# Performance work log

Measured on AMD Instinct MI355X. Metric: run time of the kernel, lower is better.

The kernel has to match this reference:

```python
import jax, jax.numpy as jnp
import numpy as np

B, S, D_IN, D_OUT, H = 4, 2048, 1024, 1024, 16
HD = D_OUT // H


def setup_inputs() -> dict:
    key = jax.random.key(0)
    ks = jax.random.split(key, 6)
    s = 1.0 / np.sqrt(D_IN)
    x = jax.random.normal(ks[0], (B, S, D_IN), dtype=jnp.float32)
    Wq = jax.random.uniform(ks[1], (D_OUT, D_IN), jnp.float32, -s, s)  # torch Linear weight [out,in]
    Wk = jax.random.uniform(ks[2], (D_OUT, D_IN), jnp.float32, -s, s)
    Wv = jax.random.uniform(ks[3], (D_OUT, D_IN), jnp.float32, -s, s)
    so = 1.0 / np.sqrt(D_OUT)
    Wo = jax.random.uniform(ks[4], (D_OUT, D_OUT), jnp.float32, -so, so)
    bo = jax.random.uniform(ks[5], (D_OUT,), jnp.float32, -so, so)
    return {"x": x, "Wq": Wq, "Wk": Wk, "Wv": Wv, "Wo": Wo, "bo": bo}


def reference(x, Wq, Wk, Wv, Wo, bo):
    b, n, _ = x.shape
    # projections (torch Linear: x @ W^T), split heads -> [b, h, n, hd]
    def heads(y):
        return y.reshape(b, n, H, HD).transpose(0, 2, 1, 3)
    q = heads(x @ Wq.T)
    k = heads(x @ Wk.T)
    v = heads(x @ Wv.T)
    scores = jnp.einsum('bhqd,bhkd->bhqk', q, k)
    causal = jnp.triu(jnp.ones((n, n), dtype=bool), k=1)
    scores = jnp.where(causal, -jnp.inf, scores)
    attn = jax.nn.softmax(scores / np.sqrt(HD), axis=-1)  # dropout p=0.0 -> identity
    ctx = jnp.einsum('bhqk,bhkd->bhqd', attn, v)
    ctx = ctx.transpose(0, 2, 1, 3).reshape(b, n, D_OUT)
    return ctx @ Wo.T + bo
```

## Files before the change

kernel.cpp:

```cpp
#include <hip/hip_runtime.h>
#include <hip/hip_bf16.h>
#include <stdint.h>

#define B_N 4
#define SEQ 2048
#define DMODEL 1024
#define NHEAD 16
#define HDIM 64
#define BHEADS (B_N * NHEAD)
#define MROWS (B_N * SEQ)

typedef short bf16x8_t __attribute__((ext_vector_type(8)));
typedef float f32x4_t __attribute__((ext_vector_type(4)));

static __device__ __forceinline__ unsigned short f2bf(float f) {
  __hip_bfloat16 h = __float2bfloat16(f);
  return __builtin_bit_cast(unsigned short, h);
}

#define GLDS16(gp, lp)                                                        \
  __builtin_amdgcn_global_load_lds(                                           \
      (const __attribute__((address_space(1))) unsigned int*)(gp),            \
      (__attribute__((address_space(3))) unsigned int*)(lp), 16, 0, 0)

__global__ void cast_f32_bf16_v4(const float* __restrict__ in,
                                 unsigned short* __restrict__ out, int n4,
                                 float scale) {
  int i = blockIdx.x * blockDim.x + threadIdx.x;
  if (i >= n4) return;
  float4 v = reinterpret_cast<const float4*>(in)[i];
  ushort4 o;
  o.x = f2bf(v.x * scale); o.y = f2bf(v.y * scale);
  o.z = f2bf(v.z * scale); o.w = f2bf(v.w * scale);
  reinterpret_cast<ushort4*>(out)[i] = o;
}

__global__ void cast_weights(const float* __restrict__ Wq,
                             const float* __restrict__ Wk,
                             const float* __restrict__ Wv,
                             const float* __restrict__ Wo,
                             unsigned short* __restrict__ out) {
  int i = blockIdx.x * blockDim.x + threadIdx.x;
  int mat = i >> 18;
  int off = i & 262143;
  const float* src = (mat == 0) ? Wq : (mat == 1) ? Wk : (mat == 2) ? Wv : Wo;
  float scale = (mat == 0) ? 0.125f : 1.0f;
  float4 v = reinterpret_cast<const float4*>(src)[off];
  ushort4 o;
  o.x = f2bf(v.x * scale); o.y = f2bf(v.y * scale);
  o.z = f2bf(v.z * scale); o.w = f2bf(v.w * scale);
  reinterpret_cast<ushort4*>(out)[i] = o;
}

__global__ __launch_bounds__(256, 2)
void gemm_qkv(const unsigned short* __restrict__ A,
              const unsigned short* __restrict__ W,
              unsigned short* __restrict__ Out) {
  __shared__ __align__(16) unsigned short smem[18432];
  unsigned short* As = smem;
  unsigned short* Bs = smem + 4096;

  const int t = threadIdx.x;
  const int lane = t & 63;
  const int w = t >> 6;
  const int quad = lane >> 4;
  const int l16 = lane & 15;
  const int rowBase = blockIdx.x * 128;
  const int colBase = blockIdx.y * 128;
  const int mat = colBase >> 10;
  const int nl = colBase & 1023;
  const int wr = (w >> 1) * 64;
  const int wc = (w & 1) * 64;
  const int K = DMODEL;

  f32x4_t zero4 = {0.f, 0.f, 0.f, 0.f};
  f32x4_t acc[4][4];
#pragma unroll
  for (int i = 0; i < 4; i++)
#pragma unroll
    for (int j = 0; j < 4; j++) acc[i][j] = zero4;

  const int sseg = ((t & 3) ^ ((t >> 3) & 3)) * 8;
  const unsigned short* Ag0 = A + (size_t)(rowBase + (t >> 2)) * K + sseg;
  const unsigned short* Ag1 = A + (size_t)(rowBase + 64 + (t >> 2)) * K + sseg;
  const unsigned short* Bg0 = W + (size_t)(colBase + (t >> 2)) * K + sseg;
  const unsigned short* Bg1 = W + (size_t)(colBase + 64 + (t >> 2)) * K + sseg;
  char* lA0 = (char*)As + t * 16;
  char* lA1 = (char*)As + t * 16 + 4096;
  char* lB0 = (char*)Bs + t * 16;
  char* lB1 = (char*)Bs + t * 16 + 4096;

  const int qsw = (quad ^ ((l16 >> 1) & 3)) * 8;

  for (int k0 = 0; k0 < K; k0 += 32) {
    GLDS16(Ag0 + k0, lA0);
    GLDS16(Ag1 + k0, lA1);
    GLDS16(Bg0 + k0, lB0);
    GLDS16(Bg1 + k0, lB1);
    __syncthreads();

    bf16x8_t af[4], bfr[4];
#pragma unroll
    for (int rt = 0; rt < 4; rt++)
      af[rt] = *(const bf16x8_t*)((const char*)As +
                                  ((wr + rt * 16 + l16) * 32 + qsw) * 2);
#pragma unroll
    for (int ct = 0; ct < 4; ct++)
      bfr[ct] = *(const bf16x8_t*)((const char*)Bs +
                                   ((wc + ct * 16 + l16) * 32 + qsw) * 2);
#pragma unroll
    for (int rt = 0; rt < 4; rt++)
#pragma unroll
      for (int ct = 0; ct < 4; ct++)
        acc[rt][ct] = __builtin_amdgcn_mfma_f32_16x16x32_bf16(
            af[rt], bfr[ct], acc[rt][ct], 0, 0, 0);
    __syncthreads();
  }

  const int hh = (nl + wc) >> 6;
  const int bb = rowBase >> 11;

  if (mat == 2) {
    unsigned short* T = smem + w * 4608;
#pragma unroll
    for (int ct = 0; ct < 4; ct++)
#pragma unroll
      for (int rt = 0; rt < 4; rt++) {
        ushort4 pk;
        pk.x = f2bf(acc[rt][ct][0]);
        pk.y = f2bf(acc[rt][ct][1]);
        pk.z = f2bf(acc[rt][ct][2]);
        pk.w = f2bf(acc[rt][ct][3]);
        *(ushort4*)&T[(ct * 16 + l16) * 72 + rt * 16 + quad * 4] = pk;
      }
    const int srow = (rowBase & (SEQ - 1)) + wr;
    unsigned short* Cq = Out + 2 * (size_t)MROWS * DMODEL;
#pragma unroll
    for (int it = 0; it < 8; it++) {
      int nn = it * 8 + (lane >> 3);
      int sg = lane & 7;
      uint4 d = *(const uint4*)&T[nn * 72 + sg * 8];
      *(uint4*)(Cq + ((size_t)(bb * NHEAD + hh) * HDIM + nn) * SEQ + srow +
                sg * 8) = d;
    }
  } else {
    unsigned short* T = smem + w * 4608;
#pragma unroll
    for (int rt = 0; rt < 4; rt++)
#pragma unroll
      for (int ct = 0; ct < 4; ct++)
#pragma unroll
        for (int r = 0; r < 4; r++)
          T[(rt * 16 + quad * 4 + r) * 72 + ct * 16 + l16] =
              f2bf(acc[rt][ct][r]);
    unsigned short* Cq = Out + (size_t)mat * MROWS * DMODEL;
#pragma unroll
    for (int it = 0; it < 8; it++) {
      int idx = it * 64 + lane;
      int row = idx >> 3, sg = idx & 7, sgx = sg ^ (row & 7);
      uint4 d = *(const uint4*)&T[row * 72 + sgx * 8];
      int m = rowBase + wr + row;
      int s = m & (SEQ - 1), b = m >> 11;
      *(uint4*)(Cq + (((size_t)(b * NHEAD + hh)) * SEQ + s) * HDIM + sgx * 8) = d;
    }
  }
}

__global__ __launch_bounds__(256, 2)
void gemm_out(const unsigned short* __restrict__ A,
              const unsigned short* __restrict__ Bw,
              float* __restrict__ Cf, const float* __restrict__ bias) {
  __shared__ __align__(16) unsigned short smem[8192];
  unsigned short* As = smem;
  unsigned short* Bs = smem + 4096;
  const int t = threadIdx.x;
  const int lane = t & 63;
  const int w = t >> 6;
  const int quad = lane >> 4;
  const int l16 = lane & 15;
  const int rowBase = blockIdx.x * 128;
  const int colBase = blockIdx.y * 128;
  const int wr = (w >> 1) * 64;
  const int wc = (w & 1) * 64;
  const int K = DMODEL, N = DMODEL;

  f32x4_t zero4 = {0.f, 0.f, 0.f, 0.f};
  f32x4_t acc[4][4];
#pragma unroll
  for (int i = 0; i < 4; i++)
#pragma unroll
    for (int j = 0; j < 4; j++) acc[i][j] = zero4;

  const int sseg = ((t & 3) ^ ((t >> 3) & 3)) * 8;
  const unsigned short* Ag0 = A + (size_t)(rowBase + (t >> 2)) * K + sseg;
  const unsigned short* Ag1 = A + (size_t)(rowBase + 64 + (t >> 2)) * K + sseg;
  const unsigned short* Bg0 = Bw + (size_t)(colBase + (t >> 2)) * K + sseg;
  const unsigned short* Bg1 = Bw + (size_t)(colBase + 64 + (t >> 2)) * K + sseg;
  char* lA0 = (char*)As + t * 16;
  char* lA1 = (char*)As + t * 16 + 4096;
  char* lB0 = (char*)Bs + t * 16;
  char* lB1 = (char*)Bs + t * 16 + 4096;
  const int qsw = (quad ^ ((l16 >> 1) & 3)) * 8;

  for (int k0 = 0; k0 < K; k0 += 32) {
    GLDS16(Ag0 + k0, lA0);
    GLDS16(Ag1 + k0, lA1);
    GLDS16(Bg0 + k0, lB0);
    GLDS16(Bg1 + k0, lB1);
    __syncthreads();
    bf16x8_t af[4], bfr[4];
#pragma unroll
    for (int rt = 0; rt < 4; rt++)
      af[rt] = *(const bf16x8_t*)((const char*)As +
                                  ((wr + rt * 16 + l16) * 32 + qsw) * 2);
#pragma unroll
    for (int ct = 0; ct < 4; ct++)
      bfr[ct] = *(const bf16x8_t*)((const char*)Bs +
                                   ((wc + ct * 16 + l16) * 32 + qsw) * 2);
#pragma unroll
    for (int rt = 0; rt < 4; rt++)
#pragma unroll
      for (int ct = 0; ct < 4; ct++)
        acc[rt][ct] = __builtin_amdgcn_mfma_f32_16x16x32_bf16(
            af[rt], bfr[ct], acc[rt][ct], 0, 0, 0);
    __syncthreads();
  }

#pragma unroll
  for (int rt = 0; rt < 4; rt++)
#pragma unroll
    for (int ct = 0; ct < 4; ct++) {
      int n = colBase + wc + ct * 16 + l16;
      float bv = bias[n];
#pragma unroll
      for (int r = 0; r < 4; r++) {
        int m = rowBase + wr + rt * 16 + quad * 4 + r;
        Cf[(size_t)m * N + n] = acc[rt][ct][r] + bv;
      }
    }
}

__global__ __launch_bounds__(256, 3)
void attn_kernel(const unsigned short* __restrict__ Qg_,
                 const unsigned short* __restrict__ Kg_,
                 const unsigned short* __restrict__ Vtg_,
                 unsigned short* __restrict__ ctx) {
  __shared__ __align__(16) unsigned short Ks[2][4096];
  __shared__ __align__(16) unsigned short Vs[2][4096];
  __shared__ __align__(16) unsigned short Ps[4][2048];

  const int t = threadIdx.x;
  const int lane = t & 63, w = t >> 6;
  const int quad = lane >> 4, l16 = lane & 15;
  const int sw = l16 & 7;
  unsigned short* PsW = &Ps[w][0];

  const int rank = blockIdx.x;
  const int qt = 15 - (rank >> 6);
  const int bh = rank & 63;
  const int nt = 2 * qt + 2;
  const size_t base = (size_t)bh * SEQ * HDIM;

  const int r0 = t >> 3;
  const int s0 = ((t & 7) ^ (r0 & 7)) * 8;
  const int r1 = r0 + 32;

  const unsigned short* Kg = Kg_ + base;
  const unsigned short* Vg = Vtg_ + base;

  GLDS16(Kg + r0 * HDIM + s0, (char*)&Ks[0][0] + t * 16);
  GLDS16(Kg + r1 * HDIM + s0, (char*)&Ks[0][0] + t * 16 + 4096);
  GLDS16(Vg + (size_t)r0 * SEQ + s0, (char*)&Vs[0][0] + t * 16);
  GLDS16(Vg + (size_t)r1 * SEQ + s0, (char*)&Vs[0][0] + t * 16 + 4096);

  const int q0w = qt * 128 + w * 32;

  bf16x8_t qf[2][2];
#pragma unroll
  for (int q2 = 0; q2 < 2; q2++)
#pragma unroll
    for (int kh = 0; kh < 2; kh++)
      qf[q2][kh] = *(const bf16x8_t*)(Qg_ + base +
          (size_t)(q0w + q2 * 16 + l16) * HDIM + kh * 32 + quad * 8);

  float l_[2] = {0.f, 0.f};
  f32x4_t zero4 = {0.f, 0.f, 0.f, 0.f};
  f32x4_t o[2][4];
#pragma unroll
  for (int q2 = 0; q2 < 2; q2++)
#pragma unroll
    for (int dt = 0; dt < 4; dt++) o[q2][dt] = zero4;

  int buf = 0;
  for (int jt = 0; jt < nt; ++jt) {
    __syncthreads();
    if (jt + 1 < nt) {
      const unsigned short* Kg2 = Kg + (size_t)(jt + 1) * 64 * HDIM;
      const unsigned short* Vg2 = Vg + (jt + 1) * 64;
      char* kd = (char*)&Ks[buf ^ 1][0] + t * 16;
      char* vd = (char*)&Vs[buf ^ 1][0] + t * 16;
      GLDS16(Kg2 + r0 * HDIM + s0, kd);
      GLDS16(Kg2 + r1 * HDIM + s0, kd + 4096);
      GLDS16(Vg2 + (size_t)r0 * SEQ + s0, vd);
      GLDS16(Vg2 + (size_t)r1 * SEQ + s0, vd + 4096);
    }

    if (jt * 64 <= q0w + 31) {
      const unsigned short* Kb = &Ks[buf][0];
      const unsigned short* Vb = &Vs[buf][0];
      f32x4_t sc[2][4];
#pragma unroll
      for (int q2 = 0; q2 < 2; q2++)
#pragma unroll
        for (int kt = 0; kt < 4; kt++) sc[q2][kt] = zero4;

#pragma unroll
      for (int kt = 0; kt < 4; kt++)
#pragma unroll
        for (int kh = 0; kh < 2; kh++) {
          bf16x8_t kf = *(const bf16x8_t*)((const char*)Kb +
              ((kt * 16 + l16) * 64 + (((kh * 4 + quad) ^ sw) * 8)) * 2);
          sc[0][kt] = __builtin_amdgcn_mfma_f32_16x16x32_bf16(
              kf, qf[0][kh], sc[0][kt], 0, 0, 0);
          sc[1][kt] = __builtin_amdgcn_mfma_f32_16x16x32_bf16(
              kf, qf[1][kh], sc[1][kt], 0, 0, 0);
        }

      if (jt * 64 + 63 > q0w) {
#pragma unroll
        for (int q2 = 0; q2 < 2; q2++) {
          int q = q0w + q2 * 16 + l16;
#pragma unroll
          for (int kt = 0; kt < 4; kt++)
#pragma unroll
            for (int r = 0; r < 4; r++) {
              int key = jt * 64 + kt * 16 + quad * 4 + r;
              if (key > q) sc[q2][kt][r] = -3.0e38f;
            }
        }
      }

#pragma unroll
      for (int q2 = 0; q2 < 2; q2++) {
        float sum = 0.f;
#pragma unroll
        for (int kt = 0; kt < 4; kt++) {
          float p0 = __expf(sc[q2][kt][0]);
          float p1 = __expf(sc[q2][kt][1]);
          float p2 = __expf(sc[q2][kt][2]);
          float p3 = __expf(sc[q2][kt][3]);
          sum += p0 + p1 + p2 + p3;
          ushort4 pk;
          pk.x = f2bf(p0); pk.y = f2bf(p1); pk.z = f2bf(p2); pk.w = f2bf(p3);
          int u = (kt * 4 + quad) ^ ((l16 & 7) << 1);
          *(ushort4*)&PsW[q2 * 1024 + l16 * 64 + u * 4] = pk;
        }
        sum += __shfl_xor(sum, 16, 64);
        sum += __shfl_xor(sum, 32, 64);
        l_[q2] += sum;
      }

      bf16x8_t pf[2][2];
#pragma unroll
      for (int q2 = 0; q2 < 2; q2++)
#pragma unroll
        for (int kc = 0; kc < 2; kc++) {
          int u = (kc * 8 + quad * 2) ^ ((l16 & 7) << 1);
          pf[q2][kc] = *(const bf16x8_t*)&PsW[q2 * 1024 + l16 * 64 + u * 4];
        }
#pragma unroll
      for (int dt = 0; dt < 4; dt++)
#pragma unroll
        for (int kc = 0; kc < 2; kc++) {
          bf16x8_t vfrag = *(const bf16x8_t*)((const char*)Vb +
              ((dt * 16 + l16) * 64 + (((kc * 4 + quad) ^ sw) * 8)) * 2);
          o[0][dt] = __builtin_amdgcn_mfma_f32_16x16x32_bf16(
              vfrag, pf[0][kc], o[0][dt], 0, 0, 0);
          o[1][dt] = __builtin_amdgcn_mfma_f32_16x16x32_bf16(
              vfrag, pf[1][kc], o[1][dt], 0, 0, 0);
        }
    }
    buf ^= 1;
  }

  const int bidx = bh >> 4, h = bh & 15;
#pragma unroll
  for (int q2 = 0; q2 < 2; q2++) {
    float inv = 1.0f / l_[q2];
#pragma unroll
    for (int dt = 0; dt < 4; dt++) {
      ushort4 pk;
      pk.x = f2bf(o[q2][dt][0] * inv);
      pk.y = f2bf(o[q2][dt][1] * inv);
      pk.z = f2bf(o[q2][dt][2] * inv);
      pk.w = f2bf(o[q2][dt][3] * inv);
      int u = (dt * 4 + quad) ^ ((l16 & 7) << 1);
      *(ushort4*)&PsW[q2 * 1024 + l16 * 64 + u * 4] = pk;
    }
  }
  {
    int qq = lane >> 2, sg = lane & 3;
#pragma unroll
    for (int q2 = 0; q2 < 2; q2++) {
      int ua = (sg * 2) ^ ((qq & 7) << 1);
      int ub = (sg * 2 + 8) ^ ((qq & 7) << 1);
      uint4 da = *(const uint4*)&PsW[q2 * 1024 + qq * 64 + ua * 4];
      uint4 db = *(const uint4*)&PsW[q2 * 1024 + qq * 64 + ub * 4];
      size_t rowoff =
          ((size_t)(bidx * SEQ + q0w + q2 * 16 + qq)) * DMODEL + h * HDIM;
      *(uint4*)(ctx + rowoff + sg * 8) = da;
      *(uint4*)(ctx + rowoff + (sg + 4) * 8) = db;
    }
  }
}

extern "C" void kernel_launch(void* const* d_in, const int* in_sizes, int n_in,
                              void* d_out, int out_size, void* d_ws,
                              size_t ws_size, hipStream_t stream) {
  const float* x  = (const float*)d_in[0];
  const float* Wq = (const float*)d_in[1];
  const float* Wk = (const float*)d_in[2];
  const float* Wv = (const float*)d_in[3];
  const float* Wo = (const float*)d_in[4];
  const float* bo = (const float*)d_in[5];
  float* out = (float*)d_out;

  const size_t XE = (size_t)MROWS * DMODEL;
  const size_t WE = (size_t)DMODEL * DMODEL;

  unsigned short* xb   = (unsigned short*)d_ws;
  unsigned short* wqb  = xb + XE;
  unsigned short* wob  = wqb + 3 * WE;
  unsigned short* Qb   = wqb + 4 * WE;
  unsigned short* Kb   = Qb + XE;
  unsigned short* Vtb  = Kb + XE;
  unsigned short* ctxb = xb;

  cast_f32_bf16_v4<<<(int)(XE / 4 + 255) / 256, 256, 0, stream>>>(x, xb,
      (int)(XE / 4), 1.0f);
  cast_weights<<<(int)(4 * WE / 4 + 255) / 256, 256, 0, stream>>>(Wq, Wk, Wv,
      Wo, wqb);

  gemm_qkv<<<dim3(MROWS / 128, 3 * DMODEL / 128), 256, 0, stream>>>(xb, wqb, Qb);

  attn_kernel<<<dim3(1024), 256, 0, stream>>>(Qb, Kb, Vtb, ctxb);

  gemm_out<<<dim3(MROWS / 128, DMODEL / 128), 256, 0, stream>>>(ctxb, wob, out, bo);
}
```

Before: 233.7 us.

## Pipeline QKV and output GEMMs with 5-slot LDS ring and 128x256 tiles

Both projection GEMMs now use 512-thread blocks computing 128x256 tiles, and load K-slices through a 5-slot LDS ring with three slices prefetched. Explicit vmcnt waits and a single barrier per iteration replace the two __syncthreads of the old loop, and MFMA sections are raised in wave priority. The intent is to hide global-load latency behind MFMA work and cut barrier overhead. In exchange the kernels use about 120 KB of shared memory and rely on hand-counted waitcnt values, which may limit occupancy and break if the compiler reorders loads.

```diff
diff --git a/kernel.cpp b/kernel.cpp
--- a/kernel.cpp
+++ b/kernel.cpp
@@ -52,13 +52,15 @@
   reinterpret_cast<ushort4*>(out)[i] = o;
 }
 
-__global__ __launch_bounds__(256, 2)
+
+#define SLOT_B 24576
+#define NSLOT 5
+
+__global__ __launch_bounds__(512, 2)
 void gemm_qkv(const unsigned short* __restrict__ A,
               const unsigned short* __restrict__ W,
               unsigned short* __restrict__ Out) {
-  __shared__ __align__(16) unsigned short smem[18432];
-  unsigned short* As = smem;
-  unsigned short* Bs = smem + 4096;
+  __shared__ __align__(16) unsigned short smem[61440];
 
   const int t = threadIdx.x;
   const int lane = t & 63;
@@ -66,12 +68,25 @@
   const int quad = lane >> 4;
   const int l16 = lane & 15;
   const int rowBase = blockIdx.x * 128;
-  const int colBase = blockIdx.y * 128;
-  const int mat = colBase >> 10;
-  const int nl = colBase & 1023;
-  const int wr = (w >> 1) * 64;
-  const int wc = (w & 1) * 64;
+  const int colBase = blockIdx.y * 256;
+  const int wr = (w >> 2) * 64;
+  const int wc = (w & 3) * 64;
   const int K = DMODEL;
+  const int NH = K / 32;
+
+  const int srow = t >> 2;
+  const int ssw = ((t & 3) ^ ((t >> 3) & 3)) * 8;
+  const unsigned short* aB  = A + (size_t)(rowBase + srow) * K + ssw;
+  const unsigned short* b0B = W + (size_t)(colBase + srow) * K + ssw;
+  const unsigned short* b1B = W + (size_t)(colBase + 128 + srow) * K + ssw;
+
+  const int swz = (quad ^ ((l16 >> 1) & 3)) * 16;
+  int offA[4], offB[4];
+#pragma unroll
+  for (int rt = 0; rt < 4; rt++) offA[rt] = (wr + rt * 16 + l16) * 64 + swz;
+#pragma unroll
+  for (int ct = 0; ct < 4; ct++)
+    offB[ct] = 8192 + (wc + ct * 16 + l16) * 64 + swz;
 
   f32x4_t zero4 = {0.f, 0.f, 0.f, 0.f};
   f32x4_t acc[4][4];
@@ -80,43 +95,57 @@
 #pragma unroll
     for (int j = 0; j < 4; j++) acc[i][j] = zero4;
 
-  const int sseg = ((t & 3) ^ ((t >> 3) & 3)) * 8;
-  const unsigned short* Ag0 = A + (size_t)(rowBase + (t >> 2)) * K + sseg;
-  const unsigned short* Ag1 = A + (size_t)(rowBase + 64 + (t >> 2)) * K + sseg;
-  const unsigned short* Bg0 = W + (size_t)(colBase + (t >> 2)) * K + sseg;
-  const unsigned short* Bg1 = W + (size_t)(colBase + 64 + (t >> 2)) * K + sseg;
-  char* lA0 = (char*)As + t * 16;
-  char* lA1 = (char*)As + t * 16 + 4096;
-  char* lB0 = (char*)Bs + t * 16;
-  char* lB1 = (char*)Bs + t * 16 + 4096;
-
-  const int qsw = (quad ^ ((l16 >> 1) & 3)) * 8;
-
-  for (int k0 = 0; k0 < K; k0 += 32) {
-    GLDS16(Ag0 + k0, lA0);
-    GLDS16(Ag1 + k0, lA1);
-    GLDS16(Bg0 + k0, lB0);
-    GLDS16(Bg1 + k0, lB1);
-    __syncthreads();
-
+#pragma unroll
+  for (int h = 0; h < 3; ++h) {
+    char* sb = (char*)smem + h * SLOT_B;
+    GLDS16(aB + h * 32, sb + t * 16);
+    GLDS16(b0B + h * 32, sb + 8192 + t * 16);
+    GLDS16(b1B + h * 32, sb + 16384 + t * 16);
+  }
+
+  int cur = 0, nxt = 3;
+  for (int h = 0; h < NH; ++h) {
+    if (h < NH - 2)       asm volatile("s_waitcnt vmcnt(6)" ::: "memory");
+    else if (h == NH - 2) asm volatile("s_waitcnt vmcnt(3)" ::: "memory");
+    else                  asm volatile("s_waitcnt vmcnt(0)" ::: "memory");
+    __builtin_amdgcn_s_barrier();
+    asm volatile("" ::: "memory");
+
+    if (h + 3 < NH) {
+      char* sb = (char*)smem + nxt * SLOT_B;
+      GLDS16(aB + (size_t)(h + 3) * 32, sb + t * 16);
+      GLDS16(b0B + (size_t)(h + 3) * 32, sb + 8192 + t * 16);
+      GLDS16(b1B + (size_t)(h + 3) * 32, sb + 16384 + t * 16);
+    }
+
+    const char* cb = (const char*)smem + cur * SLOT_B;
     bf16x8_t af[4], bfr[4];
 #pragma unroll
     for (int rt = 0; rt < 4; rt++)
-      af[rt] = *(const bf16x8_t*)((const char*)As +
-                                  ((wr + rt * 16 + l16) * 32 + qsw) * 2);
+      af[rt] = *(const bf16x8_t*)(cb + offA[rt]);
 #pragma unroll
     for (int ct = 0; ct < 4; ct++)
-      bfr[ct] = *(const bf16x8_t*)((const char*)Bs +
-                                   ((wc + ct * 16 + l16) * 32 + qsw) * 2);
+      bfr[ct] = *(const bf16x8_t*)(cb + offB[ct]);
+
+    asm volatile("s_waitcnt lgkmcnt(0)" ::: "memory");
+    __builtin_amdgcn_sched_barrier(0);
+    __builtin_amdgcn_s_setprio(1);
 #pragma unroll
     for (int rt = 0; rt < 4; rt++)
 #pragma unroll
       for (int ct = 0; ct < 4; ct++)
         acc[rt][ct] = __builtin_amdgcn_mfma_f32_16x16x32_bf16(
             af[rt], bfr[ct], acc[rt][ct], 0, 0, 0);
-    __syncthreads();
-  }
-
+    __builtin_amdgcn_s_setprio(0);
+
+    if (++cur == NSLOT) cur = 0;
+    if (++nxt == NSLOT) nxt = 0;
+  }
+
+  __syncthreads();
+
+  const int mat = colBase >> 10;
+  const int nl = colBase & 1023;
   const int hh = (nl + wc) >> 6;
   const int bb = rowBase >> 11;
 
@@ -133,14 +162,14 @@
         pk.w = f2bf(acc[rt][ct][3]);
         *(ushort4*)&T[(ct * 16 + l16) * 72 + rt * 16 + quad * 4] = pk;
       }
-    const int srow = (rowBase & (SEQ - 1)) + wr;
+    const int srw = (rowBase & (SEQ - 1)) + wr;
     unsigned short* Cq = Out + 2 * (size_t)MROWS * DMODEL;
 #pragma unroll
     for (int it = 0; it < 8; it++) {
       int nn = it * 8 + (lane >> 3);
       int sg = lane & 7;
       uint4 d = *(const uint4*)&T[nn * 72 + sg * 8];
-      *(uint4*)(Cq + ((size_t)(bb * NHEAD + hh) * HDIM + nn) * SEQ + srow +
+      *(uint4*)(Cq + ((size_t)(bb * NHEAD + hh) * HDIM + nn) * SEQ + srw +
                 sg * 8) = d;
     }
   } else {
@@ -166,23 +195,37 @@
   }
 }
 
-__global__ __launch_bounds__(256, 2)
+__global__ __launch_bounds__(512, 2)
 void gemm_out(const unsigned short* __restrict__ A,
               const unsigned short* __restrict__ Bw,
               float* __restrict__ Cf, const float* __restrict__ bias) {
-  __shared__ __align__(16) unsigned short smem[8192];
-  unsigned short* As = smem;
-  unsigned short* Bs = smem + 4096;
+  __shared__ __align__(16) unsigned short smem[61440];
+
   const int t = threadIdx.x;
   const int lane = t & 63;
   const int w = t >> 6;
   const int quad = lane >> 4;
   const int l16 = lane & 15;
   const int rowBase = blockIdx.x * 128;
-  const int colBase = blockIdx.y * 128;
-  const int wr = (w >> 1) * 64;
-  const int wc = (w & 1) * 64;
+  const int colBase = blockIdx.y * 256;
+  const int wr = (w >> 2) * 64;
+  const int wc = (w & 3) * 64;
   const int K = DMODEL, N = DMODEL;
+  const int NH = K / 32;
+
+  const int srow = t >> 2;
+  const int ssw = ((t & 3) ^ ((t >> 3) & 3)) * 8;
+  const unsigned short* aB  = A + (size_t)(rowBase + srow) * K + ssw;
+  const unsigned short* b0B = Bw + (size_t)(colBase + srow) * K + ssw;
+  const unsigned short* b1B = Bw + (size_t)(colBase + 128 + srow) * K + ssw;
+
+  const int swz = (quad ^ ((l16 >> 1) & 3)) * 16;
+  int offA[4], offB[4];
+#pragma unroll
+  for (int rt = 0; rt < 4; rt++) offA[rt] = (wr + rt * 16 + l16) * 64 + swz;
+#pragma unroll
+  for (int ct = 0; ct < 4; ct++)
+    offB[ct] = 8192 + (wc + ct * 16 + l16) * 64 + swz;
 
   f32x4_t zero4 = {0.f, 0.f, 0.f, 0.f};
   f32x4_t acc[4][4];
@@ -191,39 +234,51 @@
 #pragma unroll
     for (int j = 0; j < 4; j++) acc[i][j] = zero4;
 
-  const int sseg = ((t & 3) ^ ((t >> 3) & 3)) * 8;
-  const unsigned short* Ag0 = A + (size_t)(rowBase + (t >> 2)) * K + sseg;
-  const unsigned short* Ag1 = A + (size_t)(rowBase + 64 + (t >> 2)) * K + sseg;
-  const unsigned short* Bg0 = Bw + (size_t)(colBase + (t >> 2)) * K + sseg;
-  const unsigned short* Bg1 = Bw + (size_t)(colBase + 64 + (t >> 2)) * K + sseg;
-  char* lA0 = (char*)As + t * 16;
-  char* lA1 = (char*)As + t * 16 + 4096;
-  char* lB0 = (char*)Bs + t * 16;
-  char* lB1 = (char*)Bs + t * 16 + 4096;
-  const int qsw = (quad ^ ((l16 >> 1) & 3)) * 8;
-
-  for (int k0 = 0; k0 < K; k0 += 32) {
-    GLDS16(Ag0 + k0, lA0);
-    GLDS16(Ag1 + k0, lA1);
-    GLDS16(Bg0 + k0, lB0);
-    GLDS16(Bg1 + k0, lB1);
-    __syncthreads();
+#pragma unroll
+  for (int h = 0; h < 3; ++h) {
+    char* sb = (char*)smem + h * SLOT_B;
+    GLDS16(aB + h * 32, sb + t * 16);
+    GLDS16(b0B + h * 32, sb + 8192 + t * 16);
+    GLDS16(b1B + h * 32, sb + 16384 + t * 16);
+  }
+
+  int cur = 0, nxt = 3;
+  for (int h = 0; h < NH; ++h) {
+    if (h < NH - 2)       asm volatile("s_waitcnt vmcnt(6)" ::: "memory");
+    else if (h == NH - 2) asm volatile("s_waitcnt vmcnt(3)" ::: "memory");
+    else                  asm volatile("s_waitcnt vmcnt(0)" ::: "memory");
+    __builtin_amdgcn_s_barrier();
+    asm volatile("" ::: "memory");
+
+    if (h + 3 < NH) {
+      char* sb = (char*)smem + nxt * SLOT_B;
+      GLDS16(aB + (size_t)(h + 3) * 32, sb + t * 16);
+      GLDS16(b0B + (size_t)(h + 3) * 32, sb + 8192 + t * 16);
+      GLDS16(b1B + (size_t)(h + 3) * 32, sb + 16384 + t * 16);
+    }
+
+    const char* cb = (const char*)smem + cur * SLOT_B;
     bf16x8_t af[4], bfr[4];
 #pragma unroll
     for (int rt = 0; rt < 4; rt++)
-      af[rt] = *(const bf16x8_t*)((const char*)As +
-                                  ((wr + rt * 16 + l16) * 32 + qsw) * 2);
+      af[rt] = *(const bf16x8_t*)(cb + offA[rt]);
 #pragma unroll
     for (int ct = 0; ct < 4; ct++)
-      bfr[ct] = *(const bf16x8_t*)((const char*)Bs +
-                                   ((wc + ct * 16 + l16) * 32 + qsw) * 2);
+      bfr[ct] = *(const bf16x8_t*)(cb + offB[ct]);
+
+    asm volatile("s_waitcnt lgkmcnt(0)" ::: "memory");
+    __builtin_amdgcn_sched_barrier(0);
+    __builtin_amdgcn_s_setprio(1);
 #pragma unroll
     for (int rt = 0; rt < 4; rt++)
 #pragma unroll
       for (int ct = 0; ct < 4; ct++)
         acc[rt][ct] = __builtin_amdgcn_mfma_f32_16x16x32_bf16(
             af[rt], bfr[ct], acc[rt][ct], 0, 0, 0);
-    __syncthreads();
+    __builtin_amdgcn_s_setprio(0);
+
+    if (++cur == NSLOT) cur = 0;
+    if (++nxt == NSLOT) nxt = 0;
   }
 
 #pragma unroll
@@ -441,9 +496,9 @@
   cast_weights<<<(int)(4 * WE / 4 + 255) / 256, 256, 0, stream>>>(Wq, Wk, Wv,
       Wo, wqb);
 
-  gemm_qkv<<<dim3(MROWS / 128, 3 * DMODEL / 128), 256, 0, stream>>>(xb, wqb, Qb);
+  gemm_qkv<<<dim3(MROWS / 128, 3 * DMODEL / 256), 512, 0, stream>>>(xb, wqb, Qb);
 
   attn_kernel<<<dim3(1024), 256, 0, stream>>>(Qb, Kb, Vtb, ctxb);
 
-  gemm_out<<<dim3(MROWS / 128, DMODEL / 128), 256, 0, stream>>>(ctxb, wob, out, bo);
-}
+  gemm_out<<<dim3(MROWS / 128, DMODEL / 256), 512, 0, stream>>>(ctxb, wob, out, bo);
+}
```

Measured after the change: 228.9 us. 1.02x faster.
